# Kernel optimization log

Hardware: AMD Instinct MI355X
Metric: run time of the kernel (lower is better)

The kernel has to match this reference:

```python
import jax, jax.numpy as jnp
import numpy as np

B = 32768
NUM_CLASS = 1000
FEATURE_DIM = 512


def setup_inputs() -> dict:
    key = jax.random.key(0)
    k1, k2, k3 = jax.random.split(key, 3)
    features = jax.random.normal(k1, (B, FEATURE_DIM), dtype=jnp.float32)
    labels = jax.random.randint(k2, (B,), 0, NUM_CLASS, dtype=jnp.int32)
    center = jax.random.normal(k3, (NUM_CLASS, FEATURE_DIM), dtype=jnp.float32)
    return {"features": features, "labels": labels, "center": center}


def reference(features, labels, center):
    C = center.shape[0]
    # ---- intra loss: per-row euclidean distance to own-class center ----
    # (equivalent to gathering dist_mat[i, labels[i]] from cdist(features, center, p=2))
    diff = features - center[labels]                      # [B, D]
    dist = jnp.sqrt(jnp.sum(diff * diff, axis=-1))        # [B]
    dist = jnp.clip(dist, 1e-12, 1e12)
    intra_loss = dist.mean()

    # ---- inter loss ----
    # torch: center.scatter_add(0, labels_rep, features) -> center_param + per-class sum
    sums = jax.ops.segment_sum(features, labels, num_segments=C)          # [C, D]
    # counts: scatter_add with index [B,1] only uses first column of ones -> class counts
    counts = jax.ops.segment_sum(jnp.ones((features.shape[0],), features.dtype),
                                 labels, num_segments=C)                  # [C]
    cen = (center + sums) / jnp.clip(counts, 1.0, None)[:, None]          # [C, D]
    # source bug: loop keeps only the LAST combination (C-2, C-1)
    d_last = jnp.sqrt(jnp.sum((cen[C - 2] - cen[C - 1]) ** 2))
    inter_loss = (2.0 / d_last) * (1.0 / (C * (C - 1)))
    return (intra_loss, inter_loss)
```

## Files before the change

kernel.cpp:

```cpp
#include <hip/hip_runtime.h>

#define B_ROWS   32768
#define NUM_CLS  1000
#define FEAT     512

#define INTER_BLOCKS    16
#define INTRA_BLOCKS    1024
#define THREADS         256
#define WAVES_PER_BLOCK 4
#define ROWS_PER_WAVE   8
#define TOTAL_WAVES     (INTRA_BLOCKS * WAVES_PER_BLOCK)
#define LABELS_PER_IB   (B_ROWS / INTER_BLOCKS)
#define LISTCAP         128

typedef float f32x4 __attribute__((ext_vector_type(4)));
typedef float f32x2 __attribute__((ext_vector_type(2)));

#define WS_INTER 4096
#define SLOT     1032

#define LOADPAIR(ROW, FA,FB,FC,FD, CA,CB,CC,CD) do {                         \
    const int _lab0 = labels[(ROW)];                                         \
    const int _lab1 = labels[(ROW) + 1];                                     \
    const f32x4* _f0 = (const f32x4*)(features + (size_t)(ROW) * FEAT);      \
    const f32x4* _f1 = (const f32x4*)(features + (size_t)((ROW)+1) * FEAT);  \
    const f32x4* _c0 = (const f32x4*)(center + (size_t)_lab0 * FEAT);        \
    const f32x4* _c1 = (const f32x4*)(center + (size_t)_lab1 * FEAT);        \
    FA = _f0[lane]; FB = _f0[lane + 64];                                     \
    FC = _f1[lane]; FD = _f1[lane + 64];                                     \
    CA = _c0[lane]; CB = _c0[lane + 64];                                     \
    CC = _c1[lane]; CD = _c1[lane + 64];                                     \
} while (0)

#define REDUCE2(FA,FB,FC,FD, CA,CB,CC,CD) ({                                 \
    f32x4 _d0 = FA - CA, _d1 = FB - CB, _d2 = FC - CC, _d3 = FD - CD;        \
    float _p0 = _d0.x*_d0.x + _d0.y*_d0.y + _d0.z*_d0.z + _d0.w*_d0.w        \
              + _d1.x*_d1.x + _d1.y*_d1.y + _d1.z*_d1.z + _d1.w*_d1.w;       \
    float _p1 = _d2.x*_d2.x + _d2.y*_d2.y + _d2.z*_d2.z + _d2.w*_d2.w        \
              + _d3.x*_d3.x + _d3.y*_d3.y + _d3.z*_d3.z + _d3.w*_d3.w;       \
    const bool _b0 = lane & 1;                                               \
    float _send = _b0 ? _p0 : _p1;                                           \
    float _keep = _b0 ? _p1 : _p0;                                           \
    float _u = _keep + __shfl_xor(_send, 1);                                 \
    _u += __shfl_xor(_u, 2);                                                 \
    _u += __shfl_xor(_u, 4);                                                 \
    _u += __shfl_xor(_u, 8);                                                 \
    _u += __shfl_xor(_u, 16);                                                \
    _u += __shfl_xor(_u, 32);                                                \
    float _dist = sqrtf(_u);                                                 \
    _dist = fminf(fmaxf(_dist, 1e-12f), 1e12f);                              \
    _dist + __shfl_xor(_dist, 1);                                            \
})

__global__ __launch_bounds__(THREADS, 4) void loss_pass1(
    const float* __restrict__ features,
    const int*   __restrict__ labels,
    const float* __restrict__ center,
    float*       __restrict__ ws)
{
    if (blockIdx.x < INTER_BLOCKS) {
        const int ib = blockIdx.x;
        const int t  = threadIdx.x;

        __shared__ int list[LISTCAP];
        __shared__ int nm_s;
        if (t == 0) nm_s = 0;
        __syncthreads();

        const int4* lab4 = (const int4*)(labels + ib * LABELS_PER_IB);
        #pragma unroll
        for (int k = 0; k < 2; ++k) {
            const int j = t + k * 256;
            int4 L = lab4[j];
            const int row0 = ib * LABELS_PER_IB + 4 * j;
            if (L.x >= NUM_CLS - 2) { int i = atomicAdd(&nm_s, 1); if (i < LISTCAP) list[i] = (row0 << 1)       | (L.x - (NUM_CLS - 2)); }
            if (L.y >= NUM_CLS - 2) { int i = atomicAdd(&nm_s, 1); if (i < LISTCAP) list[i] = ((row0 + 1) << 1) | (L.y - (NUM_CLS - 2)); }
            if (L.z >= NUM_CLS - 2) { int i = atomicAdd(&nm_s, 1); if (i < LISTCAP) list[i] = ((row0 + 2) << 1) | (L.z - (NUM_CLS - 2)); }
            if (L.w >= NUM_CLS - 2) { int i = atomicAdd(&nm_s, 1); if (i < LISTCAP) list[i] = ((row0 + 3) << 1) | (L.w - (NUM_CLS - 2)); }
        }
        __syncthreads();
        const int nm = min(nm_s, LISTCAP);

        float s0a = 0.0f, s0b = 0.0f, s1a = 0.0f, s1b = 0.0f;
        int c0 = 0, c1 = 0;
        for (int m = 0; m < nm; ++m) {
            const int e   = list[m];
            const int row = e >> 1;
            const f32x2 v = ((const f32x2*)(features + (size_t)row * FEAT))[t];
            if (e & 1) { s1a += v.x; s1b += v.y; ++c1; }
            else       { s0a += v.x; s0b += v.y; ++c0; }
        }

        float* slot = ws + WS_INTER + ib * SLOT;
        if (t == 0) { slot[0] = (float)c0; slot[1] = (float)c1; }
        f32x2 v0; v0.x = s0a; v0.y = s0b;
        f32x2 v1; v1.x = s1a; v1.y = s1b;
        ((f32x2*)(slot + 2))[t]   = v0;
        ((f32x2*)(slot + 514))[t] = v1;
        return;
    }

    const int bid  = blockIdx.x - INTER_BLOCKS;
    const int lane = threadIdx.x & 63;
    const int wave = __builtin_amdgcn_readfirstlane(threadIdx.x >> 6);
    const int wid  = bid * WAVES_PER_BLOCK + wave;
    const int base_row = wid * ROWS_PER_WAVE;

    f32x4 fa0, fb0, fc0, fd0, ca0, cb0, cc0, cd0;
    f32x4 fa1, fb1, fc1, fd1, ca1, cb1, cc1, cd1;

    float acc;

    LOADPAIR(base_row,     fa0, fb0, fc0, fd0, ca0, cb0, cc0, cd0);
    LOADPAIR(base_row + 2, fa1, fb1, fc1, fd1, ca1, cb1, cc1, cd1);
    acc  = REDUCE2(fa0, fb0, fc0, fd0, ca0, cb0, cc0, cd0);
    LOADPAIR(base_row + 4, fa0, fb0, fc0, fd0, ca0, cb0, cc0, cd0);
    acc += REDUCE2(fa1, fb1, fc1, fd1, ca1, cb1, cc1, cd1);
    LOADPAIR(base_row + 6, fa1, fb1, fc1, fd1, ca1, cb1, cc1, cd1);
    acc += REDUCE2(fa0, fb0, fc0, fd0, ca0, cb0, cc0, cd0);
    acc += REDUCE2(fa1, fb1, fc1, fd1, ca1, cb1, cc1, cd1);

    if (lane == 0)
        ws[wid] = acc;
}

__global__ __launch_bounds__(512) void loss_pass2(
    const float* __restrict__ center,
    const float* __restrict__ ws,
    float*       __restrict__ out)
{
    const int t = threadIdx.x;

    float cnt0 = 0.0f, cnt1 = 0.0f;
    #pragma unroll
    for (int b = 0; b < INTER_BLOCKS; ++b) {
        const float* slot = ws + WS_INTER + b * SLOT;
        cnt0 += slot[0];
        cnt1 += slot[1];
    }
    cnt0 = fmaxf(cnt0, 1.0f);
    cnt1 = fmaxf(cnt1, 1.0f);

    float s0 = 0.0f, s1 = 0.0f;
    #pragma unroll
    for (int b = 0; b < INTER_BLOCKS; ++b) {
        const float* slot = ws + WS_INTER + b * SLOT;
        s0 += slot[2 + t];
        s1 += slot[514 + t];
    }

    float a  = (center[(size_t)(NUM_CLS - 2) * FEAT + t] + s0) / cnt0;
    float bb = (center[(size_t)(NUM_CLS - 1) * FEAT + t] + s1) / cnt1;
    float df = a - bb;
    float p_inter = df * df;

    const f32x4* part4 = (const f32x4*)ws;
    float p_intra = 0.0f;
    #pragma unroll
    for (int k = 0; k < 2; ++k) {
        f32x4 v = part4[t + k * 512];
        p_intra += (v.x + v.y) + (v.z + v.w);
    }

    #pragma unroll
    for (int off = 32; off; off >>= 1) {
        p_inter += __shfl_xor(p_inter, off);
        p_intra += __shfl_xor(p_intra, off);
    }

    __shared__ float si[8], sa[8];
    if ((t & 63) == 0) { si[t >> 6] = p_inter; sa[t >> 6] = p_intra; }
    __syncthreads();

    if (t == 0) {
        float s_inter = 0.0f, s_intra = 0.0f;
        #pragma unroll
        for (int i = 0; i < 8; ++i) { s_inter += si[i]; s_intra += sa[i]; }
        float d_last = sqrtf(s_inter);
        out[0] = s_intra * (1.0f / (float)B_ROWS);
        out[1] = (2.0f / d_last) * (1.0f / ((float)NUM_CLS * (float)(NUM_CLS - 1)));
    }
}

extern "C" void kernel_launch(void* const* d_in, const int* in_sizes, int n_in,
                              void* d_out, int out_size, void* d_ws, size_t ws_size,
                              hipStream_t stream) {
    const float* features = (const float*)d_in[0];
    const int*   labels   = (const int*)d_in[1];
    const float* center   = (const float*)d_in[2];
    float* out = (float*)d_out;
    float* ws  = (float*)d_ws;

    loss_pass1<<<INTER_BLOCKS + INTRA_BLOCKS, THREADS, 0, stream>>>(features, labels, center, ws);
    loss_pass2<<<1, 512, 0, stream>>>(center, ws, out);
}
```

Baseline: 21.67 us.

## Fuse final reduction into main kernel via last-block-done atomic counter

Merges the two-kernel pipeline into a single launch. Each block publishes its partial results with agent-scope atomic stores, then increments a global counter, and the last block to arrive performs the final reduction. The intra partials are also reduced to one value per block through shared memory instead of one per wave. This removes a kernel launch and its inter-kernel gap, at the cost of a global atomic per block and relaxed-ordering assumptions. It also relies on a workspace counter that is never reset, handled with a modulo.

```diff
diff --git a/kernel.cpp b/kernel.cpp
--- a/kernel.cpp
+++ b/kernel.cpp
@@ -6,18 +6,23 @@
 
 #define INTER_BLOCKS    16
 #define INTRA_BLOCKS    1024
+#define TOTAL_BLOCKS    (INTER_BLOCKS + INTRA_BLOCKS)
 #define THREADS         256
 #define WAVES_PER_BLOCK 4
 #define ROWS_PER_WAVE   8
-#define TOTAL_WAVES     (INTRA_BLOCKS * WAVES_PER_BLOCK)
 #define LABELS_PER_IB   (B_ROWS / INTER_BLOCKS)
 #define LISTCAP         128
 
 typedef float f32x4 __attribute__((ext_vector_type(4)));
 typedef float f32x2 __attribute__((ext_vector_type(2)));
 
-#define WS_INTER 4096
+#define WS_INTRA 0
+#define WS_INTER 1024
 #define SLOT     1032
+#define WS_DONE  17536
+
+#define ASTORE(p, v) __hip_atomic_store((p), (v), __ATOMIC_RELAXED, __HIP_MEMORY_SCOPE_AGENT)
+#define ALOAD(p)     __hip_atomic_load((p), __ATOMIC_RELAXED, __HIP_MEMORY_SCOPE_AGENT)
 
 #define LOADPAIR(ROW, FA,FB,FC,FD, CA,CB,CC,CD) do {                         \
     const int _lab0 = labels[(ROW)];                                         \
@@ -52,15 +57,18 @@
     _dist + __shfl_xor(_dist, 1);                                            \
 })
 
-__global__ __launch_bounds__(THREADS, 4) void loss_pass1(
+__global__ __launch_bounds__(THREADS, 4) void loss_one(
     const float* __restrict__ features,
     const int*   __restrict__ labels,
     const float* __restrict__ center,
-    float*       __restrict__ ws)
+    float*       __restrict__ ws,
+    float*       __restrict__ out)
 {
+    const int t    = threadIdx.x;
+    const int lane = t & 63;
+
     if (blockIdx.x < INTER_BLOCKS) {
         const int ib = blockIdx.x;
-        const int t  = threadIdx.x;
 
         __shared__ int list[LISTCAP];
         __shared__ int nm_s;
@@ -92,75 +100,83 @@
         }
 
         float* slot = ws + WS_INTER + ib * SLOT;
-        if (t == 0) { slot[0] = (float)c0; slot[1] = (float)c1; }
-        f32x2 v0; v0.x = s0a; v0.y = s0b;
-        f32x2 v1; v1.x = s1a; v1.y = s1b;
-        ((f32x2*)(slot + 2))[t]   = v0;
-        ((f32x2*)(slot + 514))[t] = v1;
-        return;
-    }
-
-    const int bid  = blockIdx.x - INTER_BLOCKS;
-    const int lane = threadIdx.x & 63;
-    const int wave = __builtin_amdgcn_readfirstlane(threadIdx.x >> 6);
-    const int wid  = bid * WAVES_PER_BLOCK + wave;
-    const int base_row = wid * ROWS_PER_WAVE;
-
-    f32x4 fa0, fb0, fc0, fd0, ca0, cb0, cc0, cd0;
-    f32x4 fa1, fb1, fc1, fd1, ca1, cb1, cc1, cd1;
-
-    float acc;
-
-    LOADPAIR(base_row,     fa0, fb0, fc0, fd0, ca0, cb0, cc0, cd0);
-    LOADPAIR(base_row + 2, fa1, fb1, fc1, fd1, ca1, cb1, cc1, cd1);
-    acc  = REDUCE2(fa0, fb0, fc0, fd0, ca0, cb0, cc0, cd0);
-    LOADPAIR(base_row + 4, fa0, fb0, fc0, fd0, ca0, cb0, cc0, cd0);
-    acc += REDUCE2(fa1, fb1, fc1, fd1, ca1, cb1, cc1, cd1);
-    LOADPAIR(base_row + 6, fa1, fb1, fc1, fd1, ca1, cb1, cc1, cd1);
-    acc += REDUCE2(fa0, fb0, fc0, fd0, ca0, cb0, cc0, cd0);
-    acc += REDUCE2(fa1, fb1, fc1, fd1, ca1, cb1, cc1, cd1);
-
-    if (lane == 0)
-        ws[wid] = acc;
-}
-
-__global__ __launch_bounds__(512) void loss_pass2(
-    const float* __restrict__ center,
-    const float* __restrict__ ws,
-    float*       __restrict__ out)
-{
-    const int t = threadIdx.x;
+        if (t == 0) { ASTORE(&slot[0], (float)c0); ASTORE(&slot[1], (float)c1); }
+        ASTORE(&slot[2 + 2*t],       s0a);
+        ASTORE(&slot[2 + 2*t + 1],   s0b);
+        ASTORE(&slot[514 + 2*t],     s1a);
+        ASTORE(&slot[514 + 2*t + 1], s1b);
+    } else {
+        const int bid  = blockIdx.x - INTER_BLOCKS;
+        const int wave = __builtin_amdgcn_readfirstlane(t >> 6);
+        const int wid  = bid * WAVES_PER_BLOCK + wave;
+        const int base_row = wid * ROWS_PER_WAVE;
+
+        f32x4 fa0, fb0, fc0, fd0, ca0, cb0, cc0, cd0;
+        f32x4 fa1, fb1, fc1, fd1, ca1, cb1, cc1, cd1;
+        float acc;
+
+        LOADPAIR(base_row,     fa0, fb0, fc0, fd0, ca0, cb0, cc0, cd0);
+        LOADPAIR(base_row + 2, fa1, fb1, fc1, fd1, ca1, cb1, cc1, cd1);
+        acc  = REDUCE2(fa0, fb0, fc0, fd0, ca0, cb0, cc0, cd0);
+        LOADPAIR(base_row + 4, fa0, fb0, fc0, fd0, ca0, cb0, cc0, cd0);
+        acc += REDUCE2(fa1, fb1, fc1, fd1, ca1, cb1, cc1, cd1);
+        LOADPAIR(base_row + 6, fa1, fb1, fc1, fd1, ca1, cb1, cc1, cd1);
+        acc += REDUCE2(fa0, fb0, fc0, fd0, ca0, cb0, cc0, cd0);
+        acc += REDUCE2(fa1, fb1, fc1, fd1, ca1, cb1, cc1, cd1);
+
+        __shared__ float s[WAVES_PER_BLOCK];
+        if (lane == 0) s[wave] = acc;
+        __syncthreads();
+        if (t == 0)
+            ASTORE(&ws[WS_INTRA + bid], s[0] + s[1] + s[2] + s[3]);
+    }
+
+    asm volatile("s_waitcnt vmcnt(0)" ::: "memory");
+    __syncthreads();
+
+    __shared__ int winner_s;
+    if (t == 0) {
+        unsigned long long* done = (unsigned long long*)(ws + WS_DONE);
+        unsigned long long old = __hip_atomic_fetch_add(done, 1ULL, __ATOMIC_RELAXED,
+                                                        __HIP_MEMORY_SCOPE_AGENT);
+        winner_s = ((old % (unsigned long long)TOTAL_BLOCKS) ==
+                    (unsigned long long)(TOTAL_BLOCKS - 1)) ? 1 : 0;
+    }
+    __syncthreads();
+    if (!winner_s) return;
+
+    float p_intra = 0.0f;
+    #pragma unroll
+    for (int k = 0; k < 4; ++k)
+        p_intra += ALOAD(&ws[WS_INTRA + t + k * 256]);
 
     float cnt0 = 0.0f, cnt1 = 0.0f;
     #pragma unroll
     for (int b = 0; b < INTER_BLOCKS; ++b) {
         const float* slot = ws + WS_INTER + b * SLOT;
-        cnt0 += slot[0];
-        cnt1 += slot[1];
+        cnt0 += ALOAD(&slot[0]);
+        cnt1 += ALOAD(&slot[1]);
     }
     cnt0 = fmaxf(cnt0, 1.0f);
     cnt1 = fmaxf(cnt1, 1.0f);
 
-    float s0 = 0.0f, s1 = 0.0f;
+    float s0a = 0.0f, s0b = 0.0f, s1a = 0.0f, s1b = 0.0f;
     #pragma unroll
     for (int b = 0; b < INTER_BLOCKS; ++b) {
         const float* slot = ws + WS_INTER + b * SLOT;
-        s0 += slot[2 + t];
-        s1 += slot[514 + t];
-    }
-
-    float a  = (center[(size_t)(NUM_CLS - 2) * FEAT + t] + s0) / cnt0;
-    float bb = (center[(size_t)(NUM_CLS - 1) * FEAT + t] + s1) / cnt1;
-    float df = a - bb;
-    float p_inter = df * df;
-
-    const f32x4* part4 = (const f32x4*)ws;
-    float p_intra = 0.0f;
-    #pragma unroll
-    for (int k = 0; k < 2; ++k) {
-        f32x4 v = part4[t + k * 512];
-        p_intra += (v.x + v.y) + (v.z + v.w);
-    }
+        s0a += ALOAD(&slot[2 + 2*t]);
+        s0b += ALOAD(&slot[2 + 2*t + 1]);
+        s1a += ALOAD(&slot[514 + 2*t]);
+        s1b += ALOAD(&slot[514 + 2*t + 1]);
+    }
+
+    const int d = 2 * t;
+    float a0 = (center[(size_t)(NUM_CLS - 2) * FEAT + d]     + s0a) / cnt0;
+    float b0 = (center[(size_t)(NUM_CLS - 1) * FEAT + d]     + s1a) / cnt1;
+    float a1 = (center[(size_t)(NUM_CLS - 2) * FEAT + d + 1] + s0b) / cnt0;
+    float b1 = (center[(size_t)(NUM_CLS - 1) * FEAT + d + 1] + s1b) / cnt1;
+    float df0 = a0 - b0, df1 = a1 - b1;
+    float p_inter = df0 * df0 + df1 * df1;
 
     #pragma unroll
     for (int off = 32; off; off >>= 1) {
@@ -168,16 +184,13 @@
         p_intra += __shfl_xor(p_intra, off);
     }
 
-    __shared__ float si[8], sa[8];
-    if ((t & 63) == 0) { si[t >> 6] = p_inter; sa[t >> 6] = p_intra; }
+    __shared__ float si[4], sa[4];
+    if (lane == 0) { si[t >> 6] = p_inter; sa[t >> 6] = p_intra; }
     __syncthreads();
 
     if (t == 0) {
-        float s_inter = 0.0f, s_intra = 0.0f;
-        #pragma unroll
-        for (int i = 0; i < 8; ++i) { s_inter += si[i]; s_intra += sa[i]; }
-        float d_last = sqrtf(s_inter);
-        out[0] = s_intra * (1.0f / (float)B_ROWS);
+        float d_last = sqrtf(si[0] + si[1] + si[2] + si[3]);
+        out[0] = (sa[0] + sa[1] + sa[2] + sa[3]) * (1.0f / (float)B_ROWS);
         out[1] = (2.0f / d_last) * (1.0f / ((float)NUM_CLS * (float)(NUM_CLS - 1)));
     }
 }
@@ -191,6 +204,5 @@
     float* out = (float*)d_out;
     float* ws  = (float*)d_ws;
 
-    loss_pass1<<<INTER_BLOCKS + INTRA_BLOCKS, THREADS, 0, stream>>>(features, labels, center, ws);
-    loss_pass2<<<1, 512, 0, stream>>>(center, ws, out);
+    loss_one<<<TOTAL_BLOCKS, THREADS, 0, stream>>>(features, labels, center, ws, out);
 }
```

Result: slower. 28.80 us (+32.9%).
